# Optimization experiments

Hardware: AMD Instinct MI355X
Metric: run time of the kernel (lower is better)

Reference implementation:

```python
import jax, jax.numpy as jnp
import numpy as np

B, N, G = 32, 262144, 256


def setup_inputs() -> dict:
    key = jax.random.key(0)
    k1, k2, k3 = jax.random.split(key, 3)
    pr = jax.random.normal(k1, (B, N), dtype=jnp.float32)
    inp_means = jax.random.normal(k2, (B, G), dtype=jnp.float32)
    vr = jax.random.randint(k3, (B, N, 1), 0, G, dtype=jnp.int32)
    W = jnp.ones((2,), dtype=jnp.float32)  # hist_weight, ones initializer
    return {"pr": pr, "inp_means": inp_means, "vr": vr, "W": W}


def reference(pr, inp_means, vr, W):
    sg = jax.lax.stop_gradient
    G = inp_means.shape[1]
    v = jnp.squeeze(vr, -1)  # [B, N] int cluster ids (stop_gradient in orig; int anyway)
    p_sg = sg(pr)

    # Per-batch segmented min/max/sum/any over clusters (replaces python loop over g).
    def seg(p, psg, vi):
        mn = jnp.full((G,), jnp.inf, p.dtype).at[vi].min(psg)    # min(where(gidx, pr, inf))
        mx = jnp.full((G,), -jnp.inf, p.dtype).at[vi].max(psg)   # max(where(gidx, pr, -inf))
        sm = jnp.zeros((G,), p.dtype).at[vi].add(p)              # sum(where(gidx, pr, 0))
        any_ = jnp.zeros((G,), bool).at[vi].set(True)            # reduce_any(gidx)
        return mn, mx, sm, any_

    vmins, vmaxs, vsum, vany = jax.vmap(seg)(pr, p_sg, v)  # each [B, G]
    # Original divides sum by cast(any)->1.0 (or 0/0=nan -> 0), i.e. the group SUM.
    vmeans = jnp.where(vany, vsum, jnp.zeros((), pr.dtype))
    vmeans = (inp_means * W[0] + vmeans * W[1]) / (W[0] + W[1])

    no_scale = vmins == vmaxs  # [B, G]
    vmins_g = jnp.take_along_axis(jnp.where(no_scale, 0.0, vmins), v, axis=1)  # [B, N]
    vmaxs_g = jnp.take_along_axis(jnp.where(no_scale, 1.0, vmaxs), v, axis=1)  # [B, N]

    sort_ids = jnp.argsort(vmeans, axis=1)
    orig_ids = jnp.argsort(sort_ids, axis=1)  # inverse permutation
    vs = jnp.take_along_axis(vmeans, sort_ids, axis=1)  # [B, G]
    cd = jnp.concatenate([vs[:, :1], vs, vs[:, -1:] * 2], axis=1)  # [B, G+2]
    # conv1d with kernel ones(2)/c, VALID: out[i] = (cd[i] + cd[i+1]) / c
    f0 = (cd[:, :-2] + cd[:, 1:-1]) / 1.999  # conv(...)[:, :-1]
    f1 = (cd[:, 1:-1] + cd[:, 2:]) / 2.001   # conv(...)[:, 1:]
    f0 = jnp.take_along_axis(
        jnp.where(no_scale, 0.0, jnp.take_along_axis(f0, orig_ids, axis=1)), v, axis=1)
    f1 = jnp.take_along_axis(
        jnp.where(no_scale, 1.0, jnp.take_along_axis(f1, orig_ids, axis=1)), v, axis=1)

    tmp = (sg(pr) - sg(vmins_g)) / sg(vmaxs_g - vmins_g) * (f1 - f0) + f0  # [B, N]
    bad = jnp.isnan(tmp) | (tmp == 0.0)
    s = pr / jnp.where(bad, 1.0, tmp)  # safe denominator (grad-safe)
    scale = jnp.where(bad | jnp.isnan(s) | jnp.isinf(s), 0.0, s)
    return pr * scale
```

## Files before the change

### kernel.cpp

```cpp
#include <hip/hip_runtime.h>
#include <math.h>

#define NB 32
#define NN 262144
#define NG 256
#define NC 64
#define CH (NN/NC)
#define SC (CH/4)
#define CD 64
#define ELD (NN/CD)

__global__ __launch_bounds__(256) void k_count(const int* __restrict__ vr,
                                               unsigned* __restrict__ cnt){
  __shared__ unsigned scnt[NG];
  const int t = threadIdx.x;
  scnt[t] = 0u;
  __syncthreads();

  const int b = blockIdx.x / NC;
  const int c = blockIdx.x % NC;
  const size_t base = (size_t)b*NN + (size_t)c*CH;
  const int4* v4 = (const int4*)(vr + base);

#pragma unroll
  for (int i = 0; i < CH/1024; i++){
    int4 v = v4[i*256 + t];
    atomicAdd(&scnt[v.x], 1u);
    atomicAdd(&scnt[v.y], 1u);
    atomicAdd(&scnt[v.z], 1u);
    atomicAdd(&scnt[v.w], 1u);
  }
  __syncthreads();
  cnt[(size_t)(b*NC + c)*NG + t] = scnt[t];
}

__global__ __launch_bounds__(256) void k_offsets(unsigned* __restrict__ cnt,
                                                 unsigned* __restrict__ grpbase,
                                                 unsigned* __restrict__ grplen){
  const int b = blockIdx.x;
  const int g = threadIdx.x;

  unsigned v[NC];
#pragma unroll
  for (int c = 0; c < NC; c++) v[c] = cnt[(size_t)(b*NC + c)*NG + g];
  unsigned tot = 0;
#pragma unroll
  for (int c = 0; c < NC; c++) tot += v[c];

  __shared__ unsigned ss[NG];
  ss[g] = tot; __syncthreads();
  for (int d = 1; d < NG; d <<= 1){
    unsigned x = (g >= d) ? ss[g - d] : 0u;
    __syncthreads();
    ss[g] += x;
    __syncthreads();
  }
  unsigned base = ss[g] - tot;

  unsigned run = base;
#pragma unroll
  for (int c = 0; c < NC; c++){
    cnt[(size_t)(b*NC + c)*NG + g] = run;
    run += v[c];
  }
  grpbase[b*NG + g] = base;
  grplen [b*NG + g] = tot;
}

__global__ __launch_bounds__(256) void k_scatter(const float* __restrict__ pr,
                                                 const int* __restrict__ vr,
                                                 const unsigned* __restrict__ off,
                                                 float* __restrict__ sorted){
  __shared__ float vbuf[CH];
  __shared__ unsigned graw32[CH/4];
  __shared__ unsigned char gbuf[CH];
  __shared__ unsigned wcnt[4][NG];
  __shared__ unsigned bias[NG];
  __shared__ unsigned ss[NG];
  const int t    = threadIdx.x;
  const int lane = t & 63;
  const int w    = t >> 6;
  const int b = blockIdx.x / NC;
  const int c = blockIdx.x % NC;
  const size_t base = (size_t)b*NN + (size_t)c*CH;

#pragma unroll
  for (int k = 0; k < 4; k++) wcnt[k][t] = 0u;
  __syncthreads();

  {
    const int4* v4 = (const int4*)(vr + base + (size_t)w*SC);
#pragma unroll
    for (int i = 0; i < SC/256; i++){
      int4 v = v4[i*64 + lane];
      atomicAdd(&wcnt[w][v.x], 1u);
      atomicAdd(&wcnt[w][v.y], 1u);
      atomicAdd(&wcnt[w][v.z], 1u);
      atomicAdd(&wcnt[w][v.w], 1u);
      graw32[w*(SC/4) + i*64 + lane] =
        (unsigned)v.x | ((unsigned)v.y << 8) | ((unsigned)v.z << 16) | ((unsigned)v.w << 24);
    }
  }
  __syncthreads();

  {
    unsigned c0 = wcnt[0][t], c1 = wcnt[1][t], c2 = wcnt[2][t], c3 = wcnt[3][t];
    unsigned tot = c0 + c1 + c2 + c3;
    ss[t] = tot; __syncthreads();
    for (int d = 1; d < NG; d <<= 1){
      unsigned v = (t >= d) ? ss[t - d] : 0u;
      __syncthreads();
      ss[t] += v;
      __syncthreads();
    }
    unsigned lb = ss[t] - tot;
    wcnt[0][t] = lb;
    wcnt[1][t] = lb + c0;
    wcnt[2][t] = lb + c0 + c1;
    wcnt[3][t] = lb + c0 + c1 + c2;
    bias[t] = off[(size_t)(b*NC + c)*NG + t] - lb;
  }
  __syncthreads();

  {
    const unsigned long long below = (lane == 0) ? 0ull : ((1ull << lane) - 1ull);
    const float* psrc = pr + base + (size_t)w*SC;
    const int shft = (lane & 3) * 8;
    for (int s = 0; s < SC/64; s++){
      float p = psrc[s*64 + lane];
      unsigned packed = graw32[w*(SC/4) + s*16 + (lane >> 2)];
      int g = (int)((packed >> shft) & 255u);
      unsigned long long mask = ~0ull;
#pragma unroll
      for (int bit = 0; bit < 8; bit++){
        int bv = (g >> bit) & 1;
        unsigned long long bal = __ballot(bv);
        mask &= bv ? bal : ~bal;
      }
      int rank = __popcll(mask & below);
      unsigned old = wcnt[w][g];
      if (rank == 0) wcnt[w][g] = old + (unsigned)__popcll(mask);
      vbuf[old + (unsigned)rank] = p;
      gbuf[old + (unsigned)rank] = (unsigned char)g;
    }
  }
  __syncthreads();

  {
    float* dst = sorted + (size_t)b*NN;
    const unsigned* gbuf32 = (const unsigned*)gbuf;
#pragma unroll
    for (int k = 0; k < CH/256; k++){
      int p = k*256 + t;
      unsigned packed = gbuf32[p >> 2];
      unsigned g = (packed >> ((p & 3) * 8)) & 255u;
      dst[bias[g] + (unsigned)p] = vbuf[p];
    }
  }
}

__global__ __launch_bounds__(32) void k_sum(const float* __restrict__ sorted,
                                            const unsigned* __restrict__ grpbase,
                                            const unsigned* __restrict__ grplen,
                                            float* __restrict__ gsum,
                                            float* __restrict__ gmn,
                                            float* __restrict__ gmx){
  const int lane = threadIdx.x;
  const int b = blockIdx.x >> 3;
  const int g = ((blockIdx.x & 7) << 5) + lane;

  const unsigned base = grpbase[b*NG + g];
  const unsigned len  = grplen [b*NG + g];
  const float* sp = sorted + (size_t)b*NN + base;

  float s = 0.0f, mn = INFINITY, mx = -INFINITY;
  float A[16], C[16];
  const unsigned nfull = len >> 4;

#define LOADV(DST, K) { _Pragma("unroll") for (int j = 0; j < 16; j++) DST[j] = sp[(K)*16u + j]; }
#define CONSV(Q)      { _Pragma("unroll") for (int j = 0; j < 16; j++){ float v = Q[j]; \
                        s = __fadd_rn(s, v); mn = fminf(mn, v); mx = fmaxf(mx, v); } }

  unsigned k = 0;
  if (nfull) LOADV(A, 0)
  for (; k + 2 <= nfull; k += 2){
    LOADV(C, k + 1)
    CONSV(A)
    if (k + 2 < nfull) LOADV(A, k + 2)
    CONSV(C)
  }
  if (k < nfull) CONSV(A)
  for (unsigned i = nfull << 4; i < len; i++){
    float v = sp[i];
    s = __fadd_rn(s, v);
    mn = fminf(mn, v); mx = fmaxf(mx, v);
  }
#undef LOADV
#undef CONSV

  gsum[b*NG + g] = s;
  gmn [b*NG + g] = mn;
  gmx [b*NG + g] = mx;
}

__global__ __launch_bounds__(256) void k_pipeline(const float* __restrict__ gsum,
                                                  const float* __restrict__ gmn,
                                                  const float* __restrict__ gmx,
                                                  const float* __restrict__ inp_means,
                                                  const float* __restrict__ Wv,
                                                  float* __restrict__ params){
  const int b = blockIdx.x;
  const int g = threadIdx.x;
  __shared__ float vm[NG];
  __shared__ float vs[NG];

  const float s   = gsum[b*NG + g];
  const float mnf = gmn [b*NG + g];
  const float mxf = gmx [b*NG + g];
  const float W0 = Wv[0], W1 = Wv[1];
  float mean = __fdiv_rn(__fadd_rn(__fmul_rn(inp_means[b*NG + g], W0),
                                   __fmul_rn(s, W1)),
                         __fadd_rn(W0, W1));
  vm[g] = mean;
  __syncthreads();

  int r = 0;
  for (int j = 0; j < NG; j++){
    float x = vm[j];
    r += (x < mean) || (x == mean && j < g);
  }
  vs[r] = mean;
  __syncthreads();

  float c0 = (r == 0)    ? vs[0]                     : vs[r-1];
  float c1 = vs[r];
  float c2 = (r == NG-1) ? __fmul_rn(vs[NG-1], 2.0f) : vs[r+1];
  float f0 = __fdiv_rn(__fadd_rn(c0, c1), 1.999f);
  float f1 = __fdiv_rn(__fadd_rn(c1, c2), 2.001f);

  bool ns = (mnf == mxf);
  params[(b*4 + 0)*NG + g] = ns ? 0.0f : mnf;
  params[(b*4 + 1)*NG + g] = ns ? 1.0f : __fsub_rn(mxf, mnf);
  params[(b*4 + 2)*NG + g] = ns ? 1.0f : __fsub_rn(f1, f0);
  params[(b*4 + 3)*NG + g] = ns ? 0.0f : f0;
}

static __device__ __forceinline__ float apply_one(float p, int g,
                                                  const float* __restrict__ sp0,
                                                  const float* __restrict__ sp1,
                                                  const float* __restrict__ sp2,
                                                  const float* __restrict__ sp3){
  float t1  = __fsub_rn(p, sp0[g]);
  float t3  = __fdiv_rn(t1, sp1[g]);
  float t5  = __fmul_rn(t3, sp2[g]);
  float tmp = __fadd_rn(t5, sp3[g]);
  bool bad = __builtin_isnan(tmp) || (tmp == 0.0f);
  float s = __fdiv_rn(p, bad ? 1.0f : tmp);
  bool bad2 = bad || __builtin_isnan(s) || __builtin_isinf(s);
  float sc = bad2 ? 0.0f : s;
  return __fmul_rn(p, sc);
}

__global__ __launch_bounds__(256) void k_apply(const float* __restrict__ pr,
                                               const int* __restrict__ vr,
                                               const float* __restrict__ params,
                                               float* __restrict__ out){
  __shared__ float sp0[NG], sp1[NG], sp2[NG], sp3[NG];
  const int t = threadIdx.x;
  const int b = blockIdx.x / CD;
  const int c = blockIdx.x % CD;

  sp0[t] = params[(b*4 + 0)*NG + t];
  sp1[t] = params[(b*4 + 1)*NG + t];
  sp2[t] = params[(b*4 + 2)*NG + t];
  sp3[t] = params[(b*4 + 3)*NG + t];
  __syncthreads();

  const size_t base = (size_t)b*NN + (size_t)c*ELD;
  const float4* p4 = (const float4*)(pr + base);
  const int4*  v4 = (const int4*)(vr + base);
  float4* o4 = (float4*)(out + base);

#pragma unroll
  for (int i = 0; i < ELD/1024; i++){
    float4 p = p4[i*256 + t];
    int4   v = v4[i*256 + t];
    float4 r;
    r.x = apply_one(p.x, v.x, sp0, sp1, sp2, sp3);
    r.y = apply_one(p.y, v.y, sp0, sp1, sp2, sp3);
    r.z = apply_one(p.z, v.z, sp0, sp1, sp2, sp3);
    r.w = apply_one(p.w, v.w, sp0, sp1, sp2, sp3);
    o4[i*256 + t] = r;
  }
}

extern "C" void kernel_launch(void* const* d_in, const int* in_sizes, int n_in,
                              void* d_out, int out_size, void* d_ws, size_t ws_size,
                              hipStream_t stream){
  const float* pr        = (const float*)d_in[0];
  const float* inp_means = (const float*)d_in[1];
  const int*   vr        = (const int*)d_in[2];
  const float* W         = (const float*)d_in[3];
  float* out = (float*)d_out;

  char* ws = (char*)d_ws;
  size_t o = 0;
  unsigned* cnt     = (unsigned*)(ws + o); o += (size_t)NB*NC*NG*4;
  unsigned* grpbase = (unsigned*)(ws + o); o += (size_t)NB*NG*4;
  unsigned* grplen  = (unsigned*)(ws + o); o += (size_t)NB*NG*4;
  float*    gsum    = (float*)   (ws + o); o += (size_t)NB*NG*4;
  float*    gmn     = (float*)   (ws + o); o += (size_t)NB*NG*4;
  float*    gmx     = (float*)   (ws + o); o += (size_t)NB*NG*4;
  float*    params  = (float*)   (ws + o); o += (size_t)NB*NG*16;
  float* sorted = out;

  k_count   <<<NB*NC, 256, 0, stream>>>(vr, cnt);
  k_offsets <<<NB,     NG, 0, stream>>>(cnt, grpbase, grplen);
  k_scatter <<<NB*NC, 256, 0, stream>>>(pr, vr, cnt, sorted);
  k_sum     <<<NB*8,   32, 0, stream>>>(sorted, grpbase, grplen, gsum, gmn, gmx);
  k_pipeline<<<NB,     NG, 0, stream>>>(gsum, gmn, gmx, inp_means, W, params);
  k_apply   <<<NB*CD, 256, 0, stream>>>(pr, vr, params, out);
}
```

Before: 182.7 us.

## Double chunk count, stream offsets via separate buffer, deepen k_sum prefetch

Doubles the number of chunks per batch row (NC 64->128), so count and scatter launch twice as many blocks, each with half the elements and half the shared-memory footprint. To cope with NC=128, k_offsets no longer holds all per-chunk counts in registers: it reads counts in groups of eight and writes the prefix offsets to a new separate buffer, re-reading cnt for the second pass. k_sum moves from a two-buffer to a four-buffer register prefetch to keep more loads in flight per group. The trade-off is more blocks and per-chunk histogram traffic, extra global reads in k_offsets, and higher register pressure in k_sum.

New measurement: 185.0 us. Within noise of the previous version (+1.3%).

```diff
diff --git a/kernel.cpp b/kernel.cpp
--- a/kernel.cpp
+++ b/kernel.cpp
@@ -4,7 +4,7 @@
 #define NB 32
 #define NN 262144
 #define NG 256
-#define NC 64
+#define NC 128
 #define CH (NN/NC)
 #define SC (CH/4)
 #define CD 64
@@ -34,18 +34,25 @@
   cnt[(size_t)(b*NC + c)*NG + t] = scnt[t];
 }
 
-__global__ __launch_bounds__(256) void k_offsets(unsigned* __restrict__ cnt,
+__global__ __launch_bounds__(256) void k_offsets(const unsigned* __restrict__ cnt,
+                                                 unsigned* __restrict__ off,
                                                  unsigned* __restrict__ grpbase,
                                                  unsigned* __restrict__ grplen){
   const int b = blockIdx.x;
   const int g = threadIdx.x;
 
-  unsigned v[NC];
-#pragma unroll
-  for (int c = 0; c < NC; c++) v[c] = cnt[(size_t)(b*NC + c)*NG + g];
   unsigned tot = 0;
-#pragma unroll
-  for (int c = 0; c < NC; c++) tot += v[c];
+  for (int c0 = 0; c0 < NC; c0 += 8){
+    unsigned v0 = cnt[(size_t)(b*NC + c0 + 0)*NG + g];
+    unsigned v1 = cnt[(size_t)(b*NC + c0 + 1)*NG + g];
+    unsigned v2 = cnt[(size_t)(b*NC + c0 + 2)*NG + g];
+    unsigned v3 = cnt[(size_t)(b*NC + c0 + 3)*NG + g];
+    unsigned v4 = cnt[(size_t)(b*NC + c0 + 4)*NG + g];
+    unsigned v5 = cnt[(size_t)(b*NC + c0 + 5)*NG + g];
+    unsigned v6 = cnt[(size_t)(b*NC + c0 + 6)*NG + g];
+    unsigned v7 = cnt[(size_t)(b*NC + c0 + 7)*NG + g];
+    tot += v0 + v1 + v2 + v3 + v4 + v5 + v6 + v7;
+  }
 
   __shared__ unsigned ss[NG];
   ss[g] = tot; __syncthreads();
@@ -58,10 +65,15 @@
   unsigned base = ss[g] - tot;
 
   unsigned run = base;
-#pragma unroll
-  for (int c = 0; c < NC; c++){
-    cnt[(size_t)(b*NC + c)*NG + g] = run;
-    run += v[c];
+  for (int c0 = 0; c0 < NC; c0 += 8){
+    unsigned v[8];
+#pragma unroll
+    for (int j = 0; j < 8; j++) v[j] = cnt[(size_t)(b*NC + c0 + j)*NG + g];
+#pragma unroll
+    for (int j = 0; j < 8; j++){
+      off[(size_t)(b*NC + c0 + j)*NG + g] = run;
+      run += v[j];
+    }
   }
   grpbase[b*NG + g] = base;
   grplen [b*NG + g] = tot;
@@ -174,22 +186,30 @@
   const float* sp = sorted + (size_t)b*NN + base;
 
   float s = 0.0f, mn = INFINITY, mx = -INFINITY;
-  float A[16], C[16];
+  float b0[16], b1[16], b2[16], b3[16];
   const unsigned nfull = len >> 4;
 
 #define LOADV(DST, K) { _Pragma("unroll") for (int j = 0; j < 16; j++) DST[j] = sp[(K)*16u + j]; }
 #define CONSV(Q)      { _Pragma("unroll") for (int j = 0; j < 16; j++){ float v = Q[j]; \
                         s = __fadd_rn(s, v); mn = fminf(mn, v); mx = fmaxf(mx, v); } }
 
+  if (nfull > 0) LOADV(b0, 0)
+  if (nfull > 1) LOADV(b1, 1)
+  if (nfull > 2) LOADV(b2, 2)
+  if (nfull > 3) LOADV(b3, 3)
   unsigned k = 0;
-  if (nfull) LOADV(A, 0)
-  for (; k + 2 <= nfull; k += 2){
-    LOADV(C, k + 1)
-    CONSV(A)
-    if (k + 2 < nfull) LOADV(A, k + 2)
-    CONSV(C)
-  }
-  if (k < nfull) CONSV(A)
+  for (; k + 4 <= nfull; k += 4){
+    CONSV(b0) if (k + 4 < nfull) LOADV(b0, k + 4)
+    CONSV(b1) if (k + 5 < nfull) LOADV(b1, k + 5)
+    CONSV(b2) if (k + 6 < nfull) LOADV(b2, k + 6)
+    CONSV(b3) if (k + 7 < nfull) LOADV(b3, k + 7)
+  }
+  {
+    unsigned r = nfull - k;
+    if (r > 0) CONSV(b0)
+    if (r > 1) CONSV(b1)
+    if (r > 2) CONSV(b2)
+  }
   for (unsigned i = nfull << 4; i < len; i++){
     float v = sp[i];
     s = __fadd_rn(s, v);
@@ -306,6 +326,7 @@
   char* ws = (char*)d_ws;
   size_t o = 0;
   unsigned* cnt     = (unsigned*)(ws + o); o += (size_t)NB*NC*NG*4;
+  unsigned* off     = (unsigned*)(ws + o); o += (size_t)NB*NC*NG*4;
   unsigned* grpbase = (unsigned*)(ws + o); o += (size_t)NB*NG*4;
   unsigned* grplen  = (unsigned*)(ws + o); o += (size_t)NB*NG*4;
   float*    gsum    = (float*)   (ws + o); o += (size_t)NB*NG*4;
@@ -315,8 +336,8 @@
   float* sorted = out;
 
   k_count   <<<NB*NC, 256, 0, stream>>>(vr, cnt);
-  k_offsets <<<NB,     NG, 0, stream>>>(cnt, grpbase, grplen);
-  k_scatter <<<NB*NC, 256, 0, stream>>>(pr, vr, cnt, sorted);
+  k_offsets <<<NB,     NG, 0, stream>>>(cnt, off, grpbase, grplen);
+  k_scatter <<<NB*NC, 256, 0, stream>>>(pr, vr, off, sorted);
   k_sum     <<<NB*8,   32, 0, stream>>>(sorted, grpbase, grplen, gsum, gmn, gmx);
   k_pipeline<<<NB,     NG, 0, stream>>>(gsum, gmn, gmx, inp_means, W, params);
   k_apply   <<<NB*CD, 256, 0, stream>>>(pr, vr, params, out);
```

## Pack group ids to bytes once and deepen vectorized loads in group reduction

Applied to the files above, without the earlier changes.

k_count now writes a byte-packed copy of the int32 group ids to workspace, and k_scatter and k_apply read that 8 MB buffer instead of the 32 MB int32 input. This cuts global memory traffic for the two later passes at the cost of an extra write in k_count. k_sum is rewritten to align to 16 bytes, use float4 loads, and keep eight buffers of loads in flight to raise memory-level parallelism per thread. The extra register use may reduce occupancy.

Result: faster. 175.2 us (-4.1%).

```diff
diff --git a/kernel.cpp b/kernel.cpp
--- a/kernel.cpp
+++ b/kernel.cpp
@@ -11,7 +11,8 @@
 #define ELD (NN/CD)
 
 __global__ __launch_bounds__(256) void k_count(const int* __restrict__ vr,
-                                               unsigned* __restrict__ cnt){
+                                               unsigned* __restrict__ cnt,
+                                               unsigned* __restrict__ gid32){
   __shared__ unsigned scnt[NG];
   const int t = threadIdx.x;
   scnt[t] = 0u;
@@ -29,6 +30,8 @@
     atomicAdd(&scnt[v.y], 1u);
     atomicAdd(&scnt[v.z], 1u);
     atomicAdd(&scnt[v.w], 1u);
+    gid32[(base >> 2) + i*256 + t] =
+      (unsigned)v.x | ((unsigned)v.y << 8) | ((unsigned)v.z << 16) | ((unsigned)v.w << 24);
   }
   __syncthreads();
   cnt[(size_t)(b*NC + c)*NG + t] = scnt[t];
@@ -68,7 +71,7 @@
 }
 
 __global__ __launch_bounds__(256) void k_scatter(const float* __restrict__ pr,
-                                                 const int* __restrict__ vr,
+                                                 const unsigned* __restrict__ gid32,
                                                  const unsigned* __restrict__ off,
                                                  float* __restrict__ sorted){
   __shared__ float vbuf[CH];
@@ -89,17 +92,15 @@
   __syncthreads();
 
   {
-    const int4* v4 = (const int4*)(vr + base + (size_t)w*SC);
-#pragma unroll
-    for (int i = 0; i < SC/256; i++){
-      int4 v = v4[i*64 + lane];
-      atomicAdd(&wcnt[w][v.x], 1u);
-      atomicAdd(&wcnt[w][v.y], 1u);
-      atomicAdd(&wcnt[w][v.z], 1u);
-      atomicAdd(&wcnt[w][v.w], 1u);
-      graw32[w*(SC/4) + i*64 + lane] =
-        (unsigned)v.x | ((unsigned)v.y << 8) | ((unsigned)v.z << 16) | ((unsigned)v.w << 24);
-    }
+    const uint4* g4 = (const uint4*)(gid32 + (base >> 2));
+    uint4 pk = g4[w*64 + lane];
+    ((uint4*)graw32)[w*64 + lane] = pk;
+#define HIST4(P) { atomicAdd(&wcnt[w][(P) & 255u], 1u); \
+                   atomicAdd(&wcnt[w][((P) >> 8) & 255u], 1u); \
+                   atomicAdd(&wcnt[w][((P) >> 16) & 255u], 1u); \
+                   atomicAdd(&wcnt[w][(P) >> 24], 1u); }
+    HIST4(pk.x) HIST4(pk.y) HIST4(pk.z) HIST4(pk.w)
+#undef HIST4
   }
   __syncthreads();
 
@@ -174,28 +175,58 @@
   const float* sp = sorted + (size_t)b*NN + base;
 
   float s = 0.0f, mn = INFINITY, mx = -INFINITY;
-  float A[16], C[16];
-  const unsigned nfull = len >> 4;
-
-#define LOADV(DST, K) { _Pragma("unroll") for (int j = 0; j < 16; j++) DST[j] = sp[(K)*16u + j]; }
-#define CONSV(Q)      { _Pragma("unroll") for (int j = 0; j < 16; j++){ float v = Q[j]; \
-                        s = __fadd_rn(s, v); mn = fminf(mn, v); mx = fmaxf(mx, v); } }
-
+
+  unsigned head = (4u - ((unsigned)(((size_t)sp) >> 2) & 3u)) & 3u;
+  if (head > len) head = len;
+  for (unsigned i = 0; i < head; i++){
+    float v = sp[i];
+    s = __fadd_rn(s, v); mn = fminf(mn, v); mx = fmaxf(mx, v);
+  }
+  const float4* f4 = (const float4*)(sp + head);
+  const unsigned rem   = len - head;
+  const unsigned nfull = rem >> 4;
+
+  float4 b0[4], b1[4], b2[4], b3[4], b4[4], b5[4], b6[4], b7[4];
+#define LOADV(D, K) { D[0]=f4[(K)*4+0]; D[1]=f4[(K)*4+1]; D[2]=f4[(K)*4+2]; D[3]=f4[(K)*4+3]; }
+#define CONS1(V)    { s=__fadd_rn(s,(V)); mn=fminf(mn,(V)); mx=fmaxf(mx,(V)); }
+#define CONSV(D)    { _Pragma("unroll") for (int j = 0; j < 4; j++){ float4 q = D[j]; \
+                      CONS1(q.x) CONS1(q.y) CONS1(q.z) CONS1(q.w) } }
+
+  if (nfull > 0) LOADV(b0, 0)
+  if (nfull > 1) LOADV(b1, 1)
+  if (nfull > 2) LOADV(b2, 2)
+  if (nfull > 3) LOADV(b3, 3)
+  if (nfull > 4) LOADV(b4, 4)
+  if (nfull > 5) LOADV(b5, 5)
+  if (nfull > 6) LOADV(b6, 6)
+  if (nfull > 7) LOADV(b7, 7)
   unsigned k = 0;
-  if (nfull) LOADV(A, 0)
-  for (; k + 2 <= nfull; k += 2){
-    LOADV(C, k + 1)
-    CONSV(A)
-    if (k + 2 < nfull) LOADV(A, k + 2)
-    CONSV(C)
-  }
-  if (k < nfull) CONSV(A)
-  for (unsigned i = nfull << 4; i < len; i++){
+  for (; k + 8 <= nfull; k += 8){
+    CONSV(b0) if (k +  8 < nfull) LOADV(b0, k +  8)
+    CONSV(b1) if (k +  9 < nfull) LOADV(b1, k +  9)
+    CONSV(b2) if (k + 10 < nfull) LOADV(b2, k + 10)
+    CONSV(b3) if (k + 11 < nfull) LOADV(b3, k + 11)
+    CONSV(b4) if (k + 12 < nfull) LOADV(b4, k + 12)
+    CONSV(b5) if (k + 13 < nfull) LOADV(b5, k + 13)
+    CONSV(b6) if (k + 14 < nfull) LOADV(b6, k + 14)
+    CONSV(b7) if (k + 15 < nfull) LOADV(b7, k + 15)
+  }
+  {
+    unsigned r = nfull - k;
+    if (r > 0) CONSV(b0)
+    if (r > 1) CONSV(b1)
+    if (r > 2) CONSV(b2)
+    if (r > 3) CONSV(b3)
+    if (r > 4) CONSV(b4)
+    if (r > 5) CONSV(b5)
+    if (r > 6) CONSV(b6)
+  }
+  for (unsigned i = head + (nfull << 4); i < len; i++){
     float v = sp[i];
-    s = __fadd_rn(s, v);
-    mn = fminf(mn, v); mx = fmaxf(mx, v);
+    s = __fadd_rn(s, v); mn = fminf(mn, v); mx = fmaxf(mx, v);
   }
 #undef LOADV
+#undef CONS1
 #undef CONSV
 
   gsum[b*NG + g] = s;
@@ -245,7 +276,7 @@
   params[(b*4 + 3)*NG + g] = ns ? 0.0f : f0;
 }
 
-static __device__ __forceinline__ float apply_one(float p, int g,
+static __device__ __forceinline__ float apply_one(float p, unsigned g,
                                                   const float* __restrict__ sp0,
                                                   const float* __restrict__ sp1,
                                                   const float* __restrict__ sp2,
@@ -262,7 +293,7 @@
 }
 
 __global__ __launch_bounds__(256) void k_apply(const float* __restrict__ pr,
-                                               const int* __restrict__ vr,
+                                               const unsigned* __restrict__ gid32,
                                                const float* __restrict__ params,
                                                float* __restrict__ out){
   __shared__ float sp0[NG], sp1[NG], sp2[NG], sp3[NG];
@@ -278,18 +309,17 @@
 
   const size_t base = (size_t)b*NN + (size_t)c*ELD;
   const float4* p4 = (const float4*)(pr + base);
-  const int4*  v4 = (const int4*)(vr + base);
   float4* o4 = (float4*)(out + base);
 
 #pragma unroll
   for (int i = 0; i < ELD/1024; i++){
     float4 p = p4[i*256 + t];
-    int4   v = v4[i*256 + t];
+    unsigned pk = gid32[(base >> 2) + i*256 + t];
     float4 r;
-    r.x = apply_one(p.x, v.x, sp0, sp1, sp2, sp3);
-    r.y = apply_one(p.y, v.y, sp0, sp1, sp2, sp3);
-    r.z = apply_one(p.z, v.z, sp0, sp1, sp2, sp3);
-    r.w = apply_one(p.w, v.w, sp0, sp1, sp2, sp3);
+    r.x = apply_one(p.x,  pk        & 255u, sp0, sp1, sp2, sp3);
+    r.y = apply_one(p.y, (pk >>  8) & 255u, sp0, sp1, sp2, sp3);
+    r.z = apply_one(p.z, (pk >> 16) & 255u, sp0, sp1, sp2, sp3);
+    r.w = apply_one(p.w,  pk >> 24,         sp0, sp1, sp2, sp3);
     o4[i*256 + t] = r;
   }
 }
@@ -306,6 +336,7 @@
   char* ws = (char*)d_ws;
   size_t o = 0;
   unsigned* cnt     = (unsigned*)(ws + o); o += (size_t)NB*NC*NG*4;
+  unsigned* gid32   = (unsigned*)(ws + o); o += (size_t)NB*NN;
   unsigned* grpbase = (unsigned*)(ws + o); o += (size_t)NB*NG*4;
   unsigned* grplen  = (unsigned*)(ws + o); o += (size_t)NB*NG*4;
   float*    gsum    = (float*)   (ws + o); o += (size_t)NB*NG*4;
@@ -314,10 +345,10 @@
   float*    params  = (float*)   (ws + o); o += (size_t)NB*NG*16;
   float* sorted = out;
 
-  k_count   <<<NB*NC, 256, 0, stream>>>(vr, cnt);
+  k_count   <<<NB*NC, 256, 0, stream>>>(vr, cnt, gid32);
   k_offsets <<<NB,     NG, 0, stream>>>(cnt, grpbase, grplen);
-  k_scatter <<<NB*NC, 256, 0, stream>>>(pr, vr, cnt, sorted);
+  k_scatter <<<NB*NC, 256, 0, stream>>>(pr, gid32, cnt, sorted);
   k_sum     <<<NB*8,   32, 0, stream>>>(sorted, grpbase, grplen, gsum, gmn, gmx);
   k_pipeline<<<NB,     NG, 0, stream>>>(gsum, gmn, gmx, inp_means, W, params);
-  k_apply   <<<NB*CD, 256, 0, stream>>>(pr, vr, params, out);
-}
+  k_apply   <<<NB*CD, 256, 0, stream>>>(pr, gid32, params, out);
+}
```
